# Optimization experiments

Hardware: AMD Instinct MI355X
Metric: run time of the kernel (lower is better)

The kernel has to match this reference:

```python
import jax, jax.numpy as jnp
import numpy as np

B, S, D, H, HD, TOPK = 2, 2048, 2048, 16, 128, 256
HIDDEN = 4 * D
EPS = 1e-6


def setup_inputs() -> dict:
    key = jax.random.key(0)
    ks = jax.random.split(key, 12)
    def g(k, shape, scale):
        return jax.random.normal(k, shape, dtype=jnp.float32) * scale
    # rotary tables: freqs_cis[s, i] = (cos, sin) of s * theta_i
    theta = 1.0 / (10000.0 ** (np.arange(0, HD, 2, dtype=np.float32) / HD))  # [HD/2]
    ang = np.arange(S, dtype=np.float32)[:, None] * theta[None, :]           # [S, HD/2]
    freqs_cis = jnp.asarray(np.stack([np.cos(ang), np.sin(ang)], axis=-1))   # [S, HD/2, 2]
    return {
        "x": g(ks[0], (B, S, D), 1.0),
        "start_pos": 0,
        "freqs_cis": freqs_cis,
        "router_w": g(ks[1], (D, 1), D ** -0.5),
        "wq": g(ks[2], (D, H * HD), D ** -0.5),
        "wk": g(ks[3], (D, H * HD), D ** -0.5),
        "wv": g(ks[4], (D, H * HD), D ** -0.5),
        "wo": g(ks[5], (H * HD, D), (H * HD) ** -0.5),
        "w1": g(ks[6], (D, HIDDEN), D ** -0.5),
        "w2": g(ks[7], (HIDDEN, D), HIDDEN ** -0.5),
        "w3": g(ks[8], (D, HIDDEN), D ** -0.5),
        "attn_norm_w": jnp.ones((D,), jnp.float32),
        "ffn_norm_w": jnp.ones((D,), jnp.float32),
    }


def _rmsnorm(x, w, eps=EPS):
    return x * jax.lax.rsqrt(jnp.mean(x * x, axis=-1, keepdims=True) + eps) * w


def _rotary(q, freqs):  # q: [B,S,H,HD], freqs: [S,HD/2,2]
    q = q.reshape(*q.shape[:-1], HD // 2, 2)
    cos = freqs[None, :, None, :, 0]
    sin = freqs[None, :, None, :, 1]
    qr = q[..., 0] * cos - q[..., 1] * sin
    qi = q[..., 0] * sin + q[..., 1] * cos
    return jnp.stack([qr, qi], axis=-1).reshape(*q.shape[:-2], HD)


def _attention(xn, freqs, tok_mask, wq, wk, wv, wo):
    b, s, _ = xn.shape
    q = (xn @ wq).reshape(b, s, H, HD)
    k = (xn @ wk).reshape(b, s, H, HD)
    v = (xn @ wv).reshape(b, s, H, HD)
    q = _rotary(q, freqs)
    k = _rotary(k, freqs)
    scores = jnp.einsum("bqhd,bkhd->bhqk", q, k) / np.sqrt(HD).astype(np.float32)
    # keys of non-selected tokens are masked out (MoD routing mask)
    scores = scores + jnp.where(tok_mask[:, None, None, :] > 0, 0.0, -1e9)
    attn = jax.nn.softmax(scores, axis=-1)
    out = jnp.einsum("bhqk,bkhd->bqhd", attn, v).reshape(b, s, H * HD)
    return out @ wo


def reference(x, start_pos, freqs_cis, router_w, wq, wk, wv, wo, w1, w2, w3, attn_norm_w, ffn_norm_w):
    b, s, _ = x.shape
    freqs = jax.lax.dynamic_slice_in_dim(freqs_cis, start_pos, s, axis=0)
    # --- router: top-k token selection + scatter mask ---
    token_weights = x @ router_w                      # [B,S,1]
    topk_vals, topk_idx = jax.lax.top_k(token_weights[..., 0], TOPK)
    mask = jnp.zeros((b, s), x.dtype).at[jnp.arange(b)[:, None], topk_idx].set(1.0)
    masked_input = x * mask[:, :, None]
    # --- dense attention + FFN on masked tokens ---
    h = masked_input + _attention(_rmsnorm(masked_input, attn_norm_w), freqs, mask, wq, wk, wv, wo)
    hn = _rmsnorm(h, ffn_norm_w)
    out = (jax.nn.silu(hn @ w1) * (hn @ w3)) @ w2    # SwiGLU FFN
    return out, token_weights, topk_idx
```

## Files before the change

kernel.cpp:

```cpp
#include <hip/hip_runtime.h>
#include <hip/hip_bf16.h>
#include <math.h>

#define B_ 2
#define S_ 2048
#define D_ 2048
#define H_ 16
#define HD_ 128
#define TOPK_ 256
#define HIDDEN_ 8192
#define EPS_ 1e-6f

constexpr int ROWS_SEL = B_ * TOPK_;
constexpr int ROWS_ALL = ROWS_SEL + B_;

typedef __attribute__((ext_vector_type(8))) short bf16x8;
typedef __attribute__((ext_vector_type(4))) float f32x4;

__device__ __forceinline__ short f2bf(float f) {
    __hip_bfloat16 h = __float2bfloat16(f);
    return *reinterpret_cast<short*>(&h);
}

__device__ __forceinline__ void gll16(const void* g, void* l) {
    __builtin_amdgcn_global_load_lds(
        (const __attribute__((address_space(1))) unsigned int*)g,
        (__attribute__((address_space(3))) unsigned int*)l, 16, 0, 0);
}

__device__ __forceinline__ float block_sum_256(float v, float* red4) {
    for (int o = 32; o; o >>= 1) v += __shfl_down(v, o);
    if ((threadIdx.x & 63) == 0) red4[threadIdx.x >> 6] = v;
    __syncthreads();
    float t = red4[0] + red4[1] + red4[2] + red4[3];
    __syncthreads();
    return t;
}

__device__ __forceinline__ float block_max_256(float v, float* red4) {
    for (int o = 32; o; o >>= 1) v = fmaxf(v, __shfl_down(v, o));
    if ((threadIdx.x & 63) == 0) red4[threadIdx.x >> 6] = v;
    __syncthreads();
    float t = fmaxf(fmaxf(red4[0], red4[1]), fmaxf(red4[2], red4[3]));
    __syncthreads();
    return t;
}

__global__ __launch_bounds__(256) void router_kernel(const float* __restrict__ x,
                                                     const float* __restrict__ rw,
                                                     float* __restrict__ tw) {
    int token = blockIdx.x;
    const float* xr = x + (long)token * D_;
    float s = 0.f;
    for (int c = threadIdx.x; c < D_; c += 256) s += xr[c] * rw[c];
    __shared__ float red4[4];
    float tot = block_sum_256(s, red4);
    if (threadIdx.x == 0) tw[token] = tot;
}

__global__ __launch_bounds__(1024) void topk_kernel(const float* __restrict__ tw,
                                                    float* __restrict__ idx_out,
                                                    int* __restrict__ sel_idx,
                                                    int* __restrict__ sel_pos) {
    int b = blockIdx.x;
    __shared__ float v[S_];
    __shared__ int id[S_];
    int t = threadIdx.x;
    for (int i = t; i < S_; i += 1024) {
        v[i] = tw[b * S_ + i];
        id[i] = i;
        sel_pos[b * S_ + i] = -1;
    }
    __syncthreads();
    for (int k = 2; k <= S_; k <<= 1) {
        for (int j = k >> 1; j > 0; j >>= 1) {
            for (int i = t; i < S_; i += 1024) {
                int ixj = i ^ j;
                if (ixj > i) {
                    float va = v[i], vb = v[ixj];
                    int ia = id[i], ib = id[ixj];
                    bool before = (va > vb) || (va == vb && ia < ib);
                    bool dir = ((i & k) == 0);
                    if (dir != before) {
                        v[i] = vb; v[ixj] = va;
                        id[i] = ib; id[ixj] = ia;
                    }
                }
            }
            __syncthreads();
        }
    }
    if (t < TOPK_) {
        idx_out[b * TOPK_ + t] = (float)id[t];
        sel_idx[b * TOPK_ + t] = id[t];
        sel_pos[b * S_ + id[t]] = t;
    }
}

__global__ __launch_bounds__(256) void gather_rmsnorm_kernel(const float* __restrict__ x,
                                                             const int* __restrict__ sel_idx,
                                                             const float* __restrict__ nw,
                                                             short* __restrict__ XN) {
    int r = blockIdx.x;
    int b = r >> 8;
    int s = sel_idx[r];
    const float* xr = x + ((long)b * S_ + s) * D_;
    __shared__ float buf[D_];
    __shared__ float red4[4];
    float ss = 0.f;
    for (int c = threadIdx.x; c < D_; c += 256) {
        float vv = xr[c];
        buf[c] = vv;
        ss += vv * vv;
    }
    float tot = block_sum_256(ss, red4);
    float scale = rsqrtf(tot / D_ + EPS_);
    for (int c = threadIdx.x; c < D_; c += 256)
        XN[(long)r * D_ + c] = f2bf(buf[c] * scale * nw[c]);
}

struct TransParams {
    const float* src[7];
    short* dst[7];
    int K[7];
    int N[7];
    int pref[8];
};

__global__ __launch_bounds__(256) void transpose_all(TransParams tp) {
    int bid = blockIdx.x;
    int w = 0;
    while (bid >= tp.pref[w + 1]) ++w;
    int local = bid - tp.pref[w];
    const float* W = tp.src[w];
    short* WT = tp.dst[w];
    int K = tp.K[w], N = tp.N[w];
    int ntiles = N >> 6;
    int n0 = (local % ntiles) * 64, k0 = (local / ntiles) * 64;

    __shared__ float L[64][65];
    int t = threadIdx.x;
    int rid = t >> 4, cid = (t & 15) * 4;
    #pragma unroll
    for (int rr = 0; rr < 4; ++rr) {
        int k = rid + rr * 16;
        float4 v = *(const float4*)&W[(size_t)(k0 + k) * N + n0 + cid];
        L[k][cid] = v.x; L[k][cid + 1] = v.y; L[k][cid + 2] = v.z; L[k][cid + 3] = v.w;
    }
    __syncthreads();
    int nid = t >> 3, kc = (t & 7) * 8;
    #pragma unroll
    for (int nn = 0; nn < 2; ++nn) {
        int n = nid + nn * 32;
        union { short s[8]; int4 v; } u;
        #pragma unroll
        for (int j = 0; j < 8; ++j) u.s[j] = f2bf(L[kc + j][n]);
        *(int4*)&WT[(size_t)(n0 + n) * K + k0 + kc] = u.v;
    }
}

__global__ __launch_bounds__(256) void gemm_mfma(
    const short* __restrict__ A,
    const short* __restrict__ B0, const short* __restrict__ B1, const short* __restrict__ B2,
    float* __restrict__ Cb, long czStride, long spStride,
    int M, int N, int Ktot, int K_per, int splits) {
    __shared__ short smem[2 * 128 * 32];
    short* As = smem;
    short* Bs = smem + 128 * 32;
    int z = blockIdx.z;
    int zmat = z / splits, sp = z % splits;
    const short* Bm = (zmat == 0) ? B0 : (zmat == 1) ? B1 : B2;
    float* C = Cb + (long)zmat * czStride + (long)sp * spStride;
    int kbase = sp * K_per;
    int row0 = blockIdx.y * 128, col0 = blockIdx.x * 128;
    int t = threadIdx.x;
    int lane = t & 63, w = t >> 6;
    int l16 = lane & 15, quad = lane >> 4;
    int wr = (w >> 1) * 64, wc = (w & 1) * 64;
    int rr = t >> 2, ch = (t & 3) * 8;
    f32x4 acc[4][4] = {};
    for (int k0 = kbase; k0 < kbase + K_per; k0 += 32) {
        __syncthreads();
        #pragma unroll
        for (int rd = 0; rd < 2; ++rd) {
            int r = rr + rd * 64;
            int ar = row0 + r; ar = (ar < M) ? ar : (M - 1);
            gll16(A + (size_t)ar * Ktot + k0 + ch, (char*)As + rd * 4096 + t * 16);
            gll16(Bm + (size_t)(col0 + r) * Ktot + k0 + ch, (char*)Bs + rd * 4096 + t * 16);
        }
        __syncthreads();
        bf16x8 af[4], bf[4];
        #pragma unroll
        for (int i = 0; i < 4; ++i)
            af[i] = *(const bf16x8*)(As + (wr + i * 16 + l16) * 32 + quad * 8);
        #pragma unroll
        for (int j = 0; j < 4; ++j)
            bf[j] = *(const bf16x8*)(Bs + (wc + j * 16 + l16) * 32 + quad * 8);
        #pragma unroll
        for (int i = 0; i < 4; ++i)
            #pragma unroll
            for (int j = 0; j < 4; ++j)
                acc[i][j] = __builtin_amdgcn_mfma_f32_16x16x32_bf16(af[i], bf[j], acc[i][j], 0, 0, 0);
    }
    #pragma unroll
    for (int i = 0; i < 4; ++i) {
        #pragma unroll
        for (int r = 0; r < 4; ++r) {
            int row = row0 + wr + i * 16 + quad * 4 + r;
            if (row < M) {
                #pragma unroll
                for (int j = 0; j < 4; ++j)
                    C[(size_t)row * N + col0 + wc + j * 16 + l16] = acc[i][j][r];
            }
        }
    }
}

template <bool BT, bool OBF>
__global__ __launch_bounds__(256) void gemm_tile(
    const float* __restrict__ A, int lda, long sAo, long sAi,
    const float* __restrict__ Bm, int ldb, long sBo, long sBi,
    void* __restrict__ Cv, int ldc, long sCo, long sCi,
    int M, int N, int K, int inner, float alpha) {
    constexpr int BM = 64, BN = 64, BK = 16, TM = 4, TN = 4;
    __shared__ float As[BK][BM + 1];
    __shared__ float Bs[BK][BN + 1];
    int z = blockIdx.z;
    const float* Ab = A + (long)(z / inner) * sAo + (long)(z % inner) * sAi;
    const float* Bb = Bm + (long)(z / inner) * sBo + (long)(z % inner) * sBi;
    long cbase = (long)(z / inner) * sCo + (long)(z % inner) * sCi;
    int row0 = blockIdx.y * BM, col0 = blockIdx.x * BN;
    int tid = threadIdx.x;
    int tx = tid % 16, ty = tid / 16;
    float acc[TM][TN] = {};
    for (int k0 = 0; k0 < K; k0 += BK) {
        {
            int kk = tid & 15;
            int rb = tid >> 4;
            #pragma unroll
            for (int j = 0; j < 4; ++j) {
                int r = rb + j * 16;
                int grow = row0 + r;
                As[kk][r] = (grow < M) ? Ab[(long)grow * lda + k0 + kk] : 0.f;
            }
        }
        if (!BT) {
            int col = tid & 63;
            int kb = tid >> 6;
            #pragma unroll
            for (int j = 0; j < 4; ++j) {
                int kk = kb + j * 4;
                Bs[kk][col] = Bb[(long)(k0 + kk) * ldb + col0 + col];
            }
        } else {
            int kk = tid & 15;
            int cb = tid >> 4;
            #pragma unroll
            for (int j = 0; j < 4; ++j) {
                int col = cb + j * 16;
                Bs[kk][col] = Bb[(long)(col0 + col) * ldb + k0 + kk];
            }
        }
        __syncthreads();
        #pragma unroll
        for (int kk = 0; kk < BK; ++kk) {
            float a[TM], bb[TN];
            #pragma unroll
            for (int i = 0; i < TM; ++i) a[i] = As[kk][ty * TM + i];
            #pragma unroll
            for (int j = 0; j < TN; ++j) bb[j] = Bs[kk][tx * TN + j];
            #pragma unroll
            for (int i = 0; i < TM; ++i)
                #pragma unroll
                for (int j = 0; j < TN; ++j) acc[i][j] += a[i] * bb[j];
        }
        __syncthreads();
    }
    #pragma unroll
    for (int i = 0; i < TM; ++i) {
        int grow = row0 + ty * TM + i;
        if (grow < M) {
            #pragma unroll
            for (int j = 0; j < TN; ++j) {
                long idx = cbase + (long)grow * ldc + col0 + tx * TN + j;
                if (OBF) ((short*)Cv)[idx] = f2bf(alpha * acc[i][j]);
                else     ((float*)Cv)[idx] = alpha * acc[i][j];
            }
        }
    }
}

__global__ __launch_bounds__(256) void qkv_finish(
    const float* __restrict__ Cp, const float* __restrict__ fc,
    const int* __restrict__ sel_idx, const int* __restrict__ sp0,
    float* __restrict__ Qf, float* __restrict__ Kf, float* __restrict__ Vf,
    int splits) {
    int r = blockIdx.x;
    int s = sel_idx[r];
    int pos = sp0[0] + s;
    const float* f = fc + (long)pos * HD_;
    const long matS = (long)ROWS_SEL * D_;
    const long spS = 3 * matS;
    const float* qp = Cp + (long)r * D_;
    const float* kp = qp + matS;
    const float* vp = qp + 2 * matS;
    for (int p = threadIdx.x; p < (D_ / 2); p += 256) {
        int h = p >> 6, d2 = p & 63;
        int e0 = h * HD_ + d2 * 2;
        float q0 = 0.f, q1 = 0.f, k0 = 0.f, k1 = 0.f, v0 = 0.f, v1 = 0.f;
        for (int sp = 0; sp < splits; ++sp) {
            long off = (long)sp * spS;
            q0 += qp[off + e0]; q1 += qp[off + e0 + 1];
            k0 += kp[off + e0]; k1 += kp[off + e0 + 1];
            v0 += vp[off + e0]; v1 += vp[off + e0 + 1];
        }
        float c = f[d2 * 2], sn = f[d2 * 2 + 1];
        Qf[(long)r * D_ + e0]     = q0 * c - q1 * sn;
        Qf[(long)r * D_ + e0 + 1] = q0 * sn + q1 * c;
        Kf[(long)r * D_ + e0]     = k0 * c - k1 * sn;
        Kf[(long)r * D_ + e0 + 1] = k0 * sn + k1 * c;
        Vf[(long)r * D_ + e0]     = v0;
        Vf[(long)r * D_ + e0 + 1] = v1;
    }
}

__global__ __launch_bounds__(256) void softmax_kernel(float* __restrict__ SC) {
    long row = blockIdx.x;
    float* p = SC + row * 256;
    int t = threadIdx.x;
    float v = p[t];
    __shared__ float red4[4];
    float m = block_max_256(v, red4);
    float e = expf(v - m);
    float s = block_sum_256(e, red4);
    p[t] = e / s;
}

__global__ __launch_bounds__(256) void vbar_kernel(const float* __restrict__ V,
                                                   short* __restrict__ Obf) {
    int b = blockIdx.y;
    int c = blockIdx.x * 256 + threadIdx.x;
    float s = 0.f;
    for (int i = 0; i < TOPK_; ++i) s += V[((long)b * TOPK_ + i) * D_ + c];
    Obf[(long)(ROWS_SEL + b) * D_ + c] = f2bf(s * (1.f / TOPK_));
}

__global__ __launch_bounds__(256) void resid_rmsnorm_kernel(const float* __restrict__ Pp,
                                                            int splits,
                                                            const float* __restrict__ x,
                                                            const int* __restrict__ sel_idx,
                                                            const float* __restrict__ nw,
                                                            short* __restrict__ HN) {
    int r = blockIdx.x;
    __shared__ float buf[D_];
    __shared__ float red4[4];
    const long spS = (long)ROWS_ALL * D_;
    const float* pr = Pp + (long)r * D_;
    const float* xr = nullptr;
    if (r < ROWS_SEL) {
        int b = r >> 8;
        int s = sel_idx[r];
        xr = x + ((long)b * S_ + s) * D_;
    }
    float ss = 0.f;
    for (int c = threadIdx.x; c < D_; c += 256) {
        float v = xr ? xr[c] : 0.f;
        for (int sp = 0; sp < splits; ++sp) v += pr[(long)sp * spS + c];
        buf[c] = v;
        ss += v * v;
    }
    float tot = block_sum_256(ss, red4);
    float scale = rsqrtf(tot / D_ + EPS_);
    for (int c = threadIdx.x; c < D_; c += 256)
        HN[(long)r * D_ + c] = f2bf(buf[c] * scale * nw[c]);
}

__global__ __launch_bounds__(256) void reduce_silu_kernel(const float* __restrict__ Gp,
                                                          short* __restrict__ FF, long n) {
    long i = (long)blockIdx.x * 256 + threadIdx.x;
    if (i < n) {
        const long cz = (long)ROWS_ALL * HIDDEN_;
        float a = Gp[i] + Gp[cz + i];
        float g = Gp[2 * cz + i] + Gp[3 * cz + i];
        FF[i] = f2bf((a / (1.f + expf(-a))) * g);
    }
}

__global__ __launch_bounds__(256) void w2_reduce_kernel(const float* __restrict__ Wp,
                                                        float* __restrict__ OUTR, long n4) {
    long i = (long)blockIdx.x * 256 + threadIdx.x;
    if (i < n4) {
        const long spS4 = (long)ROWS_ALL * D_ / 4;
        float4 s = ((const float4*)Wp)[i];
        for (int sp = 1; sp < 8; ++sp) {
            float4 v = ((const float4*)Wp)[(long)sp * spS4 + i];
            s.x += v.x; s.y += v.y; s.z += v.z; s.w += v.w;
        }
        ((float4*)OUTR)[i] = s;
    }
}

__global__ __launch_bounds__(256) void scatter_kernel(const float* __restrict__ OUTR,
                                                      const int* __restrict__ sel_pos,
                                                      float* __restrict__ out) {
    int blk = blockIdx.x;
    int b = blk >> 11;
    int p = sel_pos[blk];
    int row = (p >= 0) ? (b * TOPK_ + p) : (ROWS_SEL + b);
    const float* src = OUTR + (long)row * D_;
    float* dst = out + (long)blk * D_;
    for (int c = threadIdx.x; c < D_; c += 256) dst[c] = src[c];
}

extern "C" void kernel_launch(void* const* d_in, const int* in_sizes, int n_in,
                              void* d_out, int out_size, void* d_ws, size_t ws_size,
                              hipStream_t stream) {
    const float* x        = (const float*)d_in[0];
    const int*   startpos = (const int*)d_in[1];
    const float* freqs    = (const float*)d_in[2];
    const float* router_w = (const float*)d_in[3];
    const float* wq       = (const float*)d_in[4];
    const float* wk       = (const float*)d_in[5];
    const float* wv       = (const float*)d_in[6];
    const float* wo       = (const float*)d_in[7];
    const float* w1       = (const float*)d_in[8];
    const float* w2       = (const float*)d_in[9];
    const float* w3       = (const float*)d_in[10];
    const float* attn_w   = (const float*)d_in[11];
    const float* ffn_w    = (const float*)d_in[12];

    float* out     = (float*)d_out;
    float* tw_out  = out + (long)B_ * S_ * D_;
    float* idx_out = tw_out + (long)B_ * S_;

    char* ws = (char*)d_ws;
    auto alloc = [&](size_t bytes) -> void* {
        void* p = (void*)ws;
        ws += (bytes + 255) / 256 * 256;
        return p;
    };
    int*   sel_idx = (int*)alloc((size_t)B_ * TOPK_ * sizeof(int));
    int*   sel_pos = (int*)alloc((size_t)B_ * S_ * sizeof(int));
    short* XNbf = (short*)alloc((size_t)ROWS_SEL * D_ * sizeof(short));
    float* QKV  = (float*)alloc((size_t)3 * ROWS_SEL * D_ * sizeof(float));
    float* Qf = QKV;
    float* Kf = QKV + (size_t)ROWS_SEL * D_;
    float* Vf = QKV + (size_t)2 * ROWS_SEL * D_;
    float* SC   = (float*)alloc((size_t)B_ * H_ * TOPK_ * TOPK_ * sizeof(float));
    short* Obf  = (short*)alloc((size_t)ROWS_ALL * D_ * sizeof(short));
    short* HNbf = (short*)alloc((size_t)ROWS_ALL * D_ * sizeof(short));
    short* FFbf = (short*)alloc((size_t)ROWS_ALL * HIDDEN_ * sizeof(short));
    float* OUTR = (float*)alloc((size_t)ROWS_ALL * D_ * sizeof(float));
    float* Gar  = (float*)alloc((size_t)4 * ROWS_ALL * HIDDEN_ * sizeof(float));
    const size_t W4M = (size_t)D_ * D_;
    const size_t W16M = (size_t)D_ * HIDDEN_;
    short* WT = (short*)alloc((4 * W4M + 3 * W16M) * sizeof(short));
    short* wqT = WT;
    short* wkT = wqT + W4M;
    short* wvT = wkT + W4M;
    short* woT = wvT + W4M;
    short* w1T = woT + W4M;
    short* w3T = w1T + W16M;
    short* w2T = w3T + W16M;

    const float inv_sqrt_hd = 0.08838834764831845f;

    {
        TransParams tp;
        tp.src[0] = wq; tp.src[1] = wk; tp.src[2] = wv; tp.src[3] = wo;
        tp.src[4] = w1; tp.src[5] = w3; tp.src[6] = w2;
        tp.dst[0] = wqT; tp.dst[1] = wkT; tp.dst[2] = wvT; tp.dst[3] = woT;
        tp.dst[4] = w1T; tp.dst[5] = w3T; tp.dst[6] = w2T;
        int Ks[7] = {D_, D_, D_, D_, D_, D_, HIDDEN_};
        int Ns[7] = {D_, D_, D_, D_, HIDDEN_, HIDDEN_, D_};
        int acc = 0;
        for (int i = 0; i < 7; ++i) {
            tp.K[i] = Ks[i]; tp.N[i] = Ns[i];
            tp.pref[i] = acc;
            acc += (Ns[i] / 64) * (Ks[i] / 64);
        }
        tp.pref[7] = acc;
        transpose_all<<<acc, 256, 0, stream>>>(tp);
    }
    router_kernel<<<B_ * S_, 256, 0, stream>>>(x, router_w, tw_out);
    topk_kernel<<<B_, 1024, 0, stream>>>(tw_out, idx_out, sel_idx, sel_pos);
    gather_rmsnorm_kernel<<<ROWS_SEL, 256, 0, stream>>>(x, sel_idx, attn_w, XNbf);
    {
        dim3 g(D_ / 128, ROWS_SEL / 128, 3 * 4);
        gemm_mfma<<<g, 256, 0, stream>>>(XNbf, wqT, wkT, wvT,
                                         Gar, (long)ROWS_SEL * D_, (long)3 * ROWS_SEL * D_,
                                         ROWS_SEL, D_, D_, D_ / 4, 4);
    }
    qkv_finish<<<ROWS_SEL, 256, 0, stream>>>(Gar, freqs, sel_idx, startpos, Qf, Kf, Vf, 4);
    {
        dim3 g(TOPK_ / 64, TOPK_ / 64, B_ * H_);
        gemm_tile<true, false><<<g, 256, 0, stream>>>(
            Qf, D_, (long)TOPK_ * D_, HD_,
            Kf, D_, (long)TOPK_ * D_, HD_,
            SC, TOPK_, (long)H_ * TOPK_ * TOPK_, (long)TOPK_ * TOPK_,
            TOPK_, TOPK_, HD_, H_, inv_sqrt_hd);
    }
    softmax_kernel<<<B_ * H_ * TOPK_, 256, 0, stream>>>(SC);
    {
        dim3 g(HD_ / 64, TOPK_ / 64, B_ * H_);
        gemm_tile<false, true><<<g, 256, 0, stream>>>(
            SC, TOPK_, (long)H_ * TOPK_ * TOPK_, (long)TOPK_ * TOPK_,
            Vf, D_, (long)TOPK_ * D_, HD_,
            Obf, D_, (long)TOPK_ * D_, HD_,
            TOPK_, HD_, TOPK_, H_, 1.f);
    }
    {
        dim3 g(D_ / 256, B_, 1);
        vbar_kernel<<<g, 256, 0, stream>>>(Vf, Obf);
    }
    {
        dim3 g(D_ / 128, (ROWS_ALL + 127) / 128, 8);
        gemm_mfma<<<g, 256, 0, stream>>>(Obf, woT, woT, woT,
                                         Gar, 0, (long)ROWS_ALL * D_,
                                         ROWS_ALL, D_, D_, D_ / 8, 8);
    }
    resid_rmsnorm_kernel<<<ROWS_ALL, 256, 0, stream>>>(Gar, 8, x, sel_idx, ffn_w, HNbf);
    {
        dim3 g(HIDDEN_ / 128, (ROWS_ALL + 127) / 128, 2 * 2);
        gemm_mfma<<<g, 256, 0, stream>>>(HNbf, w1T, w3T, w3T,
                                         Gar, (long)2 * ROWS_ALL * HIDDEN_, (long)ROWS_ALL * HIDDEN_,
                                         ROWS_ALL, HIDDEN_, D_, D_ / 2, 2);
    }
    {
        long n = (long)ROWS_ALL * HIDDEN_;
        reduce_silu_kernel<<<(unsigned)((n + 255) / 256), 256, 0, stream>>>(Gar, FFbf, n);
    }
    {
        dim3 g(D_ / 128, (ROWS_ALL + 127) / 128, 8);
        gemm_mfma<<<g, 256, 0, stream>>>(FFbf, w2T, w2T, w2T,
                                         Gar, 0, (long)ROWS_ALL * D_,
                                         ROWS_ALL, D_, HIDDEN_, HIDDEN_ / 8, 8);
    }
    {
        long n4 = (long)ROWS_ALL * D_ / 4;
        w2_reduce_kernel<<<(unsigned)((n4 + 255) / 256), 256, 0, stream>>>(Gar, OUTR, n4);
    }
    scatter_kernel<<<B_ * S_, 256, 0, stream>>>(OUTR, sel_pos, out);
}
```

Baseline: 640.3 us.

## Drop weight pre-transpose, read fp32 weights in GEMM, use MFMA for attention

Removes the separate pass that transposed and converted all seven weight matrices to bf16, which read about 224MB of fp32 and wrote bf16 copies on every call. The projection GEMMs now load fp32 weight tiles straight into LDS and convert to bf16 while building MFMA fragments. The scalar attention GEMMs are replaced by bf16 MFMA kernels, with Q pre-scaled, V transposed and the softmax output stored as bf16. The router and scatter kernels are also vectorised to float4. In exchange the weight tiles now take twice the LDS and bandwidth per tile, and the strided LDS reads plus per-element conversion in the inner loop add ALU work and possible bank conflicts.

```diff
diff --git a/kernel.cpp b/kernel.cpp
--- a/kernel.cpp
+++ b/kernel.cpp
@@ -22,6 +22,12 @@
     return *reinterpret_cast<short*>(&h);
 }
 
+__device__ __forceinline__ float bf2f(short s) {
+    union { unsigned u; float f; } c;
+    c.u = ((unsigned)(unsigned short)s) << 16;
+    return c.f;
+}
+
 __device__ __forceinline__ void gll16(const void* g, void* l) {
     __builtin_amdgcn_global_load_lds(
         (const __attribute__((address_space(1))) unsigned int*)g,
@@ -50,9 +56,13 @@
                                                      const float* __restrict__ rw,
                                                      float* __restrict__ tw) {
     int token = blockIdx.x;
-    const float* xr = x + (long)token * D_;
+    const float4* xr = (const float4*)(x + (long)token * D_);
+    const float4* r4 = (const float4*)rw;
     float s = 0.f;
-    for (int c = threadIdx.x; c < D_; c += 256) s += xr[c] * rw[c];
+    for (int c = threadIdx.x; c < D_ / 4; c += 256) {
+        float4 a = xr[c], b = r4[c];
+        s += a.x * b.x + a.y * b.y + a.z * b.z + a.w * b.w;
+    }
     __shared__ float red4[4];
     float tot = block_sum_256(s, red4);
     if (threadIdx.x == 0) tw[token] = tot;
@@ -119,57 +129,16 @@
         XN[(long)r * D_ + c] = f2bf(buf[c] * scale * nw[c]);
 }
 
-struct TransParams {
-    const float* src[7];
-    short* dst[7];
-    int K[7];
-    int N[7];
-    int pref[8];
-};
-
-__global__ __launch_bounds__(256) void transpose_all(TransParams tp) {
-    int bid = blockIdx.x;
-    int w = 0;
-    while (bid >= tp.pref[w + 1]) ++w;
-    int local = bid - tp.pref[w];
-    const float* W = tp.src[w];
-    short* WT = tp.dst[w];
-    int K = tp.K[w], N = tp.N[w];
-    int ntiles = N >> 6;
-    int n0 = (local % ntiles) * 64, k0 = (local / ntiles) * 64;
-
-    __shared__ float L[64][65];
-    int t = threadIdx.x;
-    int rid = t >> 4, cid = (t & 15) * 4;
-    #pragma unroll
-    for (int rr = 0; rr < 4; ++rr) {
-        int k = rid + rr * 16;
-        float4 v = *(const float4*)&W[(size_t)(k0 + k) * N + n0 + cid];
-        L[k][cid] = v.x; L[k][cid + 1] = v.y; L[k][cid + 2] = v.z; L[k][cid + 3] = v.w;
-    }
-    __syncthreads();
-    int nid = t >> 3, kc = (t & 7) * 8;
-    #pragma unroll
-    for (int nn = 0; nn < 2; ++nn) {
-        int n = nid + nn * 32;
-        union { short s[8]; int4 v; } u;
-        #pragma unroll
-        for (int j = 0; j < 8; ++j) u.s[j] = f2bf(L[kc + j][n]);
-        *(int4*)&WT[(size_t)(n0 + n) * K + k0 + kc] = u.v;
-    }
-}
-
-__global__ __launch_bounds__(256) void gemm_mfma(
+__global__ __launch_bounds__(256) void gemm_mfma_w(
     const short* __restrict__ A,
-    const short* __restrict__ B0, const short* __restrict__ B1, const short* __restrict__ B2,
+    const float* __restrict__ B0, const float* __restrict__ B1, const float* __restrict__ B2,
     float* __restrict__ Cb, long czStride, long spStride,
     int M, int N, int Ktot, int K_per, int splits) {
-    __shared__ short smem[2 * 128 * 32];
-    short* As = smem;
-    short* Bs = smem + 128 * 32;
+    __shared__ short As[128 * 32];
+    __shared__ float Bs[32 * 128];
     int z = blockIdx.z;
     int zmat = z / splits, sp = z % splits;
-    const short* Bm = (zmat == 0) ? B0 : (zmat == 1) ? B1 : B2;
+    const float* Bm = (zmat == 0) ? B0 : (zmat == 1) ? B1 : B2;
     float* C = Cb + (long)zmat * czStride + (long)sp * spStride;
     int kbase = sp * K_per;
     int row0 = blockIdx.y * 128, col0 = blockIdx.x * 128;
@@ -177,16 +146,20 @@
     int lane = t & 63, w = t >> 6;
     int l16 = lane & 15, quad = lane >> 4;
     int wr = (w >> 1) * 64, wc = (w & 1) * 64;
-    int rr = t >> 2, ch = (t & 3) * 8;
+    int arr = t >> 2, ach = (t & 3) * 8;
+    int bkr = t >> 5, bnc = (t & 31) * 4;
     f32x4 acc[4][4] = {};
     for (int k0 = kbase; k0 < kbase + K_per; k0 += 32) {
         __syncthreads();
         #pragma unroll
         for (int rd = 0; rd < 2; ++rd) {
-            int r = rr + rd * 64;
-            int ar = row0 + r; ar = (ar < M) ? ar : (M - 1);
-            gll16(A + (size_t)ar * Ktot + k0 + ch, (char*)As + rd * 4096 + t * 16);
-            gll16(Bm + (size_t)(col0 + r) * Ktot + k0 + ch, (char*)Bs + rd * 4096 + t * 16);
+            int ar = row0 + arr + rd * 64; ar = (ar < M) ? ar : (M - 1);
+            gll16(A + (size_t)ar * Ktot + k0 + ach, (char*)As + rd * 4096 + t * 16);
+        }
+        #pragma unroll
+        for (int rd = 0; rd < 4; ++rd) {
+            int kr = k0 + rd * 8 + bkr;
+            gll16(Bm + (size_t)kr * N + col0 + bnc, (char*)Bs + rd * 4096 + t * 16);
         }
         __syncthreads();
         bf16x8 af[4], bf[4];
@@ -194,8 +167,14 @@
         for (int i = 0; i < 4; ++i)
             af[i] = *(const bf16x8*)(As + (wr + i * 16 + l16) * 32 + quad * 8);
         #pragma unroll
-        for (int j = 0; j < 4; ++j)
-            bf[j] = *(const bf16x8*)(Bs + (wc + j * 16 + l16) * 32 + quad * 8);
+        for (int j = 0; j < 4; ++j) {
+            int n = wc + j * 16 + l16;
+            union { short s[8]; bf16x8 v; } ub;
+            #pragma unroll
+            for (int jj = 0; jj < 8; ++jj)
+                ub.s[jj] = f2bf(Bs[(quad * 8 + jj) * 128 + n]);
+            bf[j] = ub.v;
+        }
         #pragma unroll
         for (int i = 0; i < 4; ++i)
             #pragma unroll
@@ -216,75 +195,62 @@
     }
 }
 
-template <bool BT, bool OBF>
-__global__ __launch_bounds__(256) void gemm_tile(
-    const float* __restrict__ A, int lda, long sAo, long sAi,
-    const float* __restrict__ Bm, int ldb, long sBo, long sBi,
-    void* __restrict__ Cv, int ldc, long sCo, long sCi,
-    int M, int N, int K, int inner, float alpha) {
-    constexpr int BM = 64, BN = 64, BK = 16, TM = 4, TN = 4;
-    __shared__ float As[BK][BM + 1];
-    __shared__ float Bs[BK][BN + 1];
+template <bool OBF>
+__global__ __launch_bounds__(256) void gemm_mfma_attn(
+    const short* __restrict__ A, long sAo, long sAi, int lda,
+    const short* __restrict__ Bm, long sBo, long sBi, int ldb,
+    void* __restrict__ Cv, long sCo, long sCi, int ldc,
+    int M, int N, int K, int inner) {
+    __shared__ short smem[2 * 128 * 32];
+    short* As = smem;
+    short* Bs = smem + 128 * 32;
     int z = blockIdx.z;
-    const float* Ab = A + (long)(z / inner) * sAo + (long)(z % inner) * sAi;
-    const float* Bb = Bm + (long)(z / inner) * sBo + (long)(z % inner) * sBi;
-    long cbase = (long)(z / inner) * sCo + (long)(z % inner) * sCi;
-    int row0 = blockIdx.y * BM, col0 = blockIdx.x * BN;
-    int tid = threadIdx.x;
-    int tx = tid % 16, ty = tid / 16;
-    float acc[TM][TN] = {};
-    for (int k0 = 0; k0 < K; k0 += BK) {
-        {
-            int kk = tid & 15;
-            int rb = tid >> 4;
+    int zo = z / inner, zi = z % inner;
+    const short* Ab = A + (long)zo * sAo + (long)zi * sAi;
+    const short* Bb = Bm + (long)zo * sBo + (long)zi * sBi;
+    long cbase = (long)zo * sCo + (long)zi * sCi;
+    int row0 = blockIdx.y * 128, col0 = blockIdx.x * 128;
+    int t = threadIdx.x;
+    int lane = t & 63, w = t >> 6;
+    int l16 = lane & 15, quad = lane >> 4;
+    int wr = (w >> 1) * 64, wc = (w & 1) * 64;
+    int rr = t >> 2, ch = (t & 3) * 8;
+    f32x4 acc[4][4] = {};
+    for (int k0 = 0; k0 < K; k0 += 32) {
+        __syncthreads();
+        #pragma unroll
+        for (int rd = 0; rd < 2; ++rd) {
+            int r = rr + rd * 64;
+            int ar = row0 + r; ar = (ar < M) ? ar : (M - 1);
+            gll16(Ab + (size_t)ar * lda + k0 + ch, (char*)As + rd * 4096 + t * 16);
+            gll16(Bb + (size_t)(col0 + r) * ldb + k0 + ch, (char*)Bs + rd * 4096 + t * 16);
+        }
+        __syncthreads();
+        bf16x8 af[4], bfr[4];
+        #pragma unroll
+        for (int i = 0; i < 4; ++i)
+            af[i] = *(const bf16x8*)(As + (wr + i * 16 + l16) * 32 + quad * 8);
+        #pragma unroll
+        for (int j = 0; j < 4; ++j)
+            bfr[j] = *(const bf16x8*)(Bs + (wc + j * 16 + l16) * 32 + quad * 8);
+        #pragma unroll
+        for (int i = 0; i < 4; ++i)
             #pragma unroll
-            for (int j = 0; j < 4; ++j) {
-                int r = rb + j * 16;
-                int grow = row0 + r;
-                As[kk][r] = (grow < M) ? Ab[(long)grow * lda + k0 + kk] : 0.f;
-            }
-        }
-        if (!BT) {
-            int col = tid & 63;
-            int kb = tid >> 6;
-            #pragma unroll
-            for (int j = 0; j < 4; ++j) {
-                int kk = kb + j * 4;
-                Bs[kk][col] = Bb[(long)(k0 + kk) * ldb + col0 + col];
-            }
-        } else {
-            int kk = tid & 15;
-            int cb = tid >> 4;
-            #pragma unroll
-            for (int j = 0; j < 4; ++j) {
-                int col = cb + j * 16;
-                Bs[kk][col] = Bb[(long)(col0 + col) * ldb + k0 + kk];
-            }
-        }
-        __syncthreads();
-        #pragma unroll
-        for (int kk = 0; kk < BK; ++kk) {
-            float a[TM], bb[TN];
-            #pragma unroll
-            for (int i = 0; i < TM; ++i) a[i] = As[kk][ty * TM + i];
-            #pragma unroll
-            for (int j = 0; j < TN; ++j) bb[j] = Bs[kk][tx * TN + j];
-            #pragma unroll
-            for (int i = 0; i < TM; ++i)
+            for (int j = 0; j < 4; ++j)
+                acc[i][j] = __builtin_amdgcn_mfma_f32_16x16x32_bf16(af[i], bfr[j], acc[i][j], 0, 0, 0);
+    }
+    #pragma unroll
+    for (int i = 0; i < 4; ++i) {
+        #pragma unroll
+        for (int r = 0; r < 4; ++r) {
+            int row = row0 + wr + i * 16 + quad * 4 + r;
+            if (row < M) {
                 #pragma unroll
-                for (int j = 0; j < TN; ++j) acc[i][j] += a[i] * bb[j];
-        }
-        __syncthreads();
-    }
-    #pragma unroll
-    for (int i = 0; i < TM; ++i) {
-        int grow = row0 + ty * TM + i;
-        if (grow < M) {
-            #pragma unroll
-            for (int j = 0; j < TN; ++j) {
-                long idx = cbase + (long)grow * ldc + col0 + tx * TN + j;
-                if (OBF) ((short*)Cv)[idx] = f2bf(alpha * acc[i][j]);
-                else     ((float*)Cv)[idx] = alpha * acc[i][j];
+                for (int j = 0; j < 4; ++j) {
+                    long idx = cbase + (size_t)row * ldc + col0 + wc + j * 16 + l16;
+                    if (OBF) ((short*)Cv)[idx] = f2bf(acc[i][j][r]);
+                    else     ((float*)Cv)[idx] = acc[i][j][r];
+                }
             }
         }
     }
@@ -293,7 +259,7 @@
 __global__ __launch_bounds__(256) void qkv_finish(
     const float* __restrict__ Cp, const float* __restrict__ fc,
     const int* __restrict__ sel_idx, const int* __restrict__ sp0,
-    float* __restrict__ Qf, float* __restrict__ Kf, float* __restrict__ Vf,
+    short* __restrict__ Qbf, short* __restrict__ Kbf, short* __restrict__ Vbf,
     int splits) {
     int r = blockIdx.x;
     int s = sel_idx[r];
@@ -304,6 +270,7 @@
     const float* qp = Cp + (long)r * D_;
     const float* kp = qp + matS;
     const float* vp = qp + 2 * matS;
+    const float qscale = 0.08838834764831845f;
     for (int p = threadIdx.x; p < (D_ / 2); p += 256) {
         int h = p >> 6, d2 = p & 63;
         int e0 = h * HD_ + d2 * 2;
@@ -315,33 +282,62 @@
             v0 += vp[off + e0]; v1 += vp[off + e0 + 1];
         }
         float c = f[d2 * 2], sn = f[d2 * 2 + 1];
-        Qf[(long)r * D_ + e0]     = q0 * c - q1 * sn;
-        Qf[(long)r * D_ + e0 + 1] = q0 * sn + q1 * c;
-        Kf[(long)r * D_ + e0]     = k0 * c - k1 * sn;
-        Kf[(long)r * D_ + e0 + 1] = k0 * sn + k1 * c;
-        Vf[(long)r * D_ + e0]     = v0;
-        Vf[(long)r * D_ + e0 + 1] = v1;
-    }
-}
-
-__global__ __launch_bounds__(256) void softmax_kernel(float* __restrict__ SC) {
+        Qbf[(long)r * D_ + e0]     = f2bf((q0 * c - q1 * sn) * qscale);
+        Qbf[(long)r * D_ + e0 + 1] = f2bf((q0 * sn + q1 * c) * qscale);
+        Kbf[(long)r * D_ + e0]     = f2bf(k0 * c - k1 * sn);
+        Kbf[(long)r * D_ + e0 + 1] = f2bf(k0 * sn + k1 * c);
+        Vbf[(long)r * D_ + e0]     = f2bf(v0);
+        Vbf[(long)r * D_ + e0 + 1] = f2bf(v1);
+    }
+}
+
+__global__ __launch_bounds__(256) void vt_kernel(const short* __restrict__ Vbf,
+                                                 short* __restrict__ VT) {
+    int z = blockIdx.z;
+    int b = z >> 4, h = z & 15;
+    int key0 = blockIdx.x * 64, d0 = blockIdx.y * 64;
+    __shared__ short L[64][72];
+    int t = threadIdx.x;
+    int kr = t >> 3, dc = (t & 7) * 8;
+    #pragma unroll
+    for (int rr = 0; rr < 2; ++rr) {
+        int key = kr + rr * 32;
+        union { short s[8]; int4 v; } u;
+        u.v = *(const int4*)&Vbf[(size_t)(b * 256 + key0 + key) * D_ + h * 128 + d0 + dc];
+        #pragma unroll
+        for (int j = 0; j < 8; ++j) L[key][dc + j] = u.s[j];
+    }
+    __syncthreads();
+    int dr = t >> 3, kc = (t & 7) * 8;
+    #pragma unroll
+    for (int rr = 0; rr < 2; ++rr) {
+        int d = dr + rr * 32;
+        union { short s[8]; int4 v; } u;
+        #pragma unroll
+        for (int j = 0; j < 8; ++j) u.s[j] = L[kc + j][d];
+        *(int4*)&VT[((size_t)z * 128 + d0 + d) * 256 + key0 + kc] = u.v;
+    }
+}
+
+__global__ __launch_bounds__(256) void softmax_kernel(const float* __restrict__ SC,
+                                                      short* __restrict__ Pbf) {
     long row = blockIdx.x;
-    float* p = SC + row * 256;
+    const float* p = SC + row * 256;
     int t = threadIdx.x;
     float v = p[t];
     __shared__ float red4[4];
     float m = block_max_256(v, red4);
     float e = expf(v - m);
     float s = block_sum_256(e, red4);
-    p[t] = e / s;
-}
-
-__global__ __launch_bounds__(256) void vbar_kernel(const float* __restrict__ V,
+    Pbf[row * 256 + t] = f2bf(e / s);
+}
+
+__global__ __launch_bounds__(256) void vbar_kernel(const short* __restrict__ Vbf,
                                                    short* __restrict__ Obf) {
     int b = blockIdx.y;
     int c = blockIdx.x * 256 + threadIdx.x;
     float s = 0.f;
-    for (int i = 0; i < TOPK_; ++i) s += V[((long)b * TOPK_ + i) * D_ + c];
+    for (int i = 0; i < TOPK_; ++i) s += bf2f(Vbf[((long)b * TOPK_ + i) * D_ + c]);
     Obf[(long)(ROWS_SEL + b) * D_ + c] = f2bf(s * (1.f / TOPK_));
 }
 
@@ -407,9 +403,9 @@
     int b = blk >> 11;
     int p = sel_pos[blk];
     int row = (p >= 0) ? (b * TOPK_ + p) : (ROWS_SEL + b);
-    const float* src = OUTR + (long)row * D_;
-    float* dst = out + (long)blk * D_;
-    for (int c = threadIdx.x; c < D_; c += 256) dst[c] = src[c];
+    const float4* src = (const float4*)(OUTR + (long)row * D_);
+    float4* dst = (float4*)(out + (long)blk * D_);
+    for (int c = threadIdx.x; c < D_ / 4; c += 256) dst[c] = src[c];
 }
 
 extern "C" void kernel_launch(void* const* d_in, const int* in_sizes, int n_in,
@@ -442,89 +438,65 @@
     int*   sel_idx = (int*)alloc((size_t)B_ * TOPK_ * sizeof(int));
     int*   sel_pos = (int*)alloc((size_t)B_ * S_ * sizeof(int));
     short* XNbf = (short*)alloc((size_t)ROWS_SEL * D_ * sizeof(short));
-    float* QKV  = (float*)alloc((size_t)3 * ROWS_SEL * D_ * sizeof(float));
-    float* Qf = QKV;
-    float* Kf = QKV + (size_t)ROWS_SEL * D_;
-    float* Vf = QKV + (size_t)2 * ROWS_SEL * D_;
+    short* Qbf  = (short*)alloc((size_t)ROWS_SEL * D_ * sizeof(short));
+    short* Kbf  = (short*)alloc((size_t)ROWS_SEL * D_ * sizeof(short));
+    short* Vbf  = (short*)alloc((size_t)ROWS_SEL * D_ * sizeof(short));
+    short* VT   = (short*)alloc((size_t)B_ * H_ * HD_ * TOPK_ * sizeof(short));
     float* SC   = (float*)alloc((size_t)B_ * H_ * TOPK_ * TOPK_ * sizeof(float));
+    short* Pbf  = (short*)alloc((size_t)B_ * H_ * TOPK_ * TOPK_ * sizeof(short));
     short* Obf  = (short*)alloc((size_t)ROWS_ALL * D_ * sizeof(short));
     short* HNbf = (short*)alloc((size_t)ROWS_ALL * D_ * sizeof(short));
     short* FFbf = (short*)alloc((size_t)ROWS_ALL * HIDDEN_ * sizeof(short));
     float* OUTR = (float*)alloc((size_t)ROWS_ALL * D_ * sizeof(float));
     float* Gar  = (float*)alloc((size_t)4 * ROWS_ALL * HIDDEN_ * sizeof(float));
-    const size_t W4M = (size_t)D_ * D_;
-    const size_t W16M = (size_t)D_ * HIDDEN_;
-    short* WT = (short*)alloc((4 * W4M + 3 * W16M) * sizeof(short));
-    short* wqT = WT;
-    short* wkT = wqT + W4M;
-    short* wvT = wkT + W4M;
-    short* woT = wvT + W4M;
-    short* w1T = woT + W4M;
-    short* w3T = w1T + W16M;
-    short* w2T = w3T + W16M;
-
-    const float inv_sqrt_hd = 0.08838834764831845f;
-
-    {
-        TransParams tp;
-        tp.src[0] = wq; tp.src[1] = wk; tp.src[2] = wv; tp.src[3] = wo;
-        tp.src[4] = w1; tp.src[5] = w3; tp.src[6] = w2;
-        tp.dst[0] = wqT; tp.dst[1] = wkT; tp.dst[2] = wvT; tp.dst[3] = woT;
-        tp.dst[4] = w1T; tp.dst[5] = w3T; tp.dst[6] = w2T;
-        int Ks[7] = {D_, D_, D_, D_, D_, D_, HIDDEN_};
-        int Ns[7] = {D_, D_, D_, D_, HIDDEN_, HIDDEN_, D_};
-        int acc = 0;
-        for (int i = 0; i < 7; ++i) {
-            tp.K[i] = Ks[i]; tp.N[i] = Ns[i];
-            tp.pref[i] = acc;
-            acc += (Ns[i] / 64) * (Ks[i] / 64);
-        }
-        tp.pref[7] = acc;
-        transpose_all<<<acc, 256, 0, stream>>>(tp);
-    }
+
     router_kernel<<<B_ * S_, 256, 0, stream>>>(x, router_w, tw_out);
     topk_kernel<<<B_, 1024, 0, stream>>>(tw_out, idx_out, sel_idx, sel_pos);
     gather_rmsnorm_kernel<<<ROWS_SEL, 256, 0, stream>>>(x, sel_idx, attn_w, XNbf);
     {
         dim3 g(D_ / 128, ROWS_SEL / 128, 3 * 4);
-        gemm_mfma<<<g, 256, 0, stream>>>(XNbf, wqT, wkT, wvT,
-                                         Gar, (long)ROWS_SEL * D_, (long)3 * ROWS_SEL * D_,
-                                         ROWS_SEL, D_, D_, D_ / 4, 4);
-    }
-    qkv_finish<<<ROWS_SEL, 256, 0, stream>>>(Gar, freqs, sel_idx, startpos, Qf, Kf, Vf, 4);
-    {
-        dim3 g(TOPK_ / 64, TOPK_ / 64, B_ * H_);
-        gemm_tile<true, false><<<g, 256, 0, stream>>>(
-            Qf, D_, (long)TOPK_ * D_, HD_,
-            Kf, D_, (long)TOPK_ * D_, HD_,
-            SC, TOPK_, (long)H_ * TOPK_ * TOPK_, (long)TOPK_ * TOPK_,
-            TOPK_, TOPK_, HD_, H_, inv_sqrt_hd);
-    }
-    softmax_kernel<<<B_ * H_ * TOPK_, 256, 0, stream>>>(SC);
-    {
-        dim3 g(HD_ / 64, TOPK_ / 64, B_ * H_);
-        gemm_tile<false, true><<<g, 256, 0, stream>>>(
-            SC, TOPK_, (long)H_ * TOPK_ * TOPK_, (long)TOPK_ * TOPK_,
-            Vf, D_, (long)TOPK_ * D_, HD_,
-            Obf, D_, (long)TOPK_ * D_, HD_,
-            TOPK_, HD_, TOPK_, H_, 1.f);
+        gemm_mfma_w<<<g, 256, 0, stream>>>(XNbf, wq, wk, wv,
+                                           Gar, (long)ROWS_SEL * D_, (long)3 * ROWS_SEL * D_,
+                                           ROWS_SEL, D_, D_, D_ / 4, 4);
+    }
+    qkv_finish<<<ROWS_SEL, 256, 0, stream>>>(Gar, freqs, sel_idx, startpos, Qbf, Kbf, Vbf, 4);
+    {
+        dim3 g(4, 2, B_ * H_);
+        vt_kernel<<<g, 256, 0, stream>>>(Vbf, VT);
+    }
+    {
+        dim3 g(2, 2, B_ * H_);
+        gemm_mfma_attn<false><<<g, 256, 0, stream>>>(
+            Qbf, (long)TOPK_ * D_, HD_, D_,
+            Kbf, (long)TOPK_ * D_, HD_, D_,
+            SC, (long)H_ * TOPK_ * TOPK_, (long)TOPK_ * TOPK_, TOPK_,
+            TOPK_, TOPK_, HD_, H_);
+    }
+    softmax_kernel<<<B_ * H_ * TOPK_, 256, 0, stream>>>(SC, Pbf);
+    {
+        dim3 g(1, 2, B_ * H_);
+        gemm_mfma_attn<true><<<g, 256, 0, stream>>>(
+            Pbf, (long)H_ * TOPK_ * TOPK_, (long)TOPK_ * TOPK_, TOPK_,
+            VT, (long)H_ * HD_ * TOPK_, (long)HD_ * TOPK_, TOPK_,
+            Obf, (long)TOPK_ * D_, HD_, D_,
+            TOPK_, HD_, TOPK_, H_);
     }
     {
         dim3 g(D_ / 256, B_, 1);
-        vbar_kernel<<<g, 256, 0, stream>>>(Vf, Obf);
+        vbar_kernel<<<g, 256, 0, stream>>>(Vbf, Obf);
     }
     {
         dim3 g(D_ / 128, (ROWS_ALL + 127) / 128, 8);
-        gemm_mfma<<<g, 256, 0, stream>>>(Obf, woT, woT, woT,
-                                         Gar, 0, (long)ROWS_ALL * D_,
-                                         ROWS_ALL, D_, D_, D_ / 8, 8);
+        gemm_mfma_w<<<g, 256, 0, stream>>>(Obf, wo, wo, wo,
+                                           Gar, 0, (long)ROWS_ALL * D_,
+                                           ROWS_ALL, D_, D_, D_ / 8, 8);
     }
     resid_rmsnorm_kernel<<<ROWS_ALL, 256, 0, stream>>>(Gar, 8, x, sel_idx, ffn_w, HNbf);
     {
         dim3 g(HIDDEN_ / 128, (ROWS_ALL + 127) / 128, 2 * 2);
-        gemm_mfma<<<g, 256, 0, stream>>>(HNbf, w1T, w3T, w3T,
-                                         Gar, (long)2 * ROWS_ALL * HIDDEN_, (long)ROWS_ALL * HIDDEN_,
-                                         ROWS_ALL, HIDDEN_, D_, D_ / 2, 2);
+        gemm_mfma_w<<<g, 256, 0, stream>>>(HNbf, w1, w3, w3,
+                                           Gar, (long)2 * ROWS_ALL * HIDDEN_, (long)ROWS_ALL * HIDDEN_,
+                                           ROWS_ALL, HIDDEN_, D_, D_ / 2, 2);
     }
     {
         long n = (long)ROWS_ALL * HIDDEN_;
@@ -532,9 +504,9 @@
     }
     {
         dim3 g(D_ / 128, (ROWS_ALL + 127) / 128, 8);
-        gemm_mfma<<<g, 256, 0, stream>>>(FFbf, w2T, w2T, w2T,
-                                         Gar, 0, (long)ROWS_ALL * D_,
-                                         ROWS_ALL, D_, HIDDEN_, HIDDEN_ / 8, 8);
+        gemm_mfma_w<<<g, 256, 0, stream>>>(FFbf, w2, w2, w2,
+                                           Gar, 0, (long)ROWS_ALL * D_,
+                                           ROWS_ALL, D_, HIDDEN_, HIDDEN_ / 8, 8);
     }
     {
         long n4 = (long)ROWS_ALL * D_ / 4;
```

After: 572.2 us. 1.12x faster.
